# Performance work log

Hardware: AMD Instinct MI355X
Metric: run time of the kernel (lower is better)

Reference implementation:

```python
import jax, jax.numpy as jnp
import numpy as np

BS, C, H, W = 128, 256, 9, 9
D = 9                      # spectral window size
PS = 15                    # padsize
PAD_SPACE = PS - H         # 6
PAD1 = D // 2              # 4 (spectral pad)
START = PAD_SPACE // 2     # 3 (output crop offset)
SPE_HEAD = 25
SHARE_HEAD = 9
SIDE = 5                   # spe_head_Sidelength
BN_EPS = 1e-5


def setup_inputs() -> dict:
    key = jax.random.key(0)
    ks = jax.random.split(key, 12)
    s = 0.1
    return {
        "x": jax.random.normal(ks[0], (BS, C, H, W), jnp.float32),
        "wk": jax.random.normal(ks[1], (H * W, 1, D), jnp.float32) * s,   # depthwise conv1d over spectral axis
        "bk": jax.random.normal(ks[2], (H * W,), jnp.float32) * s,
        "w1": jax.random.normal(ks[3], (SPE_HEAD, SHARE_HEAD, 2 * SHARE_HEAD), jnp.float32) * s,  # grouped 1x1, no bias
        "bn_gamma": jnp.ones((SPE_HEAD * SHARE_HEAD,), jnp.float32),
        "bn_beta": jnp.zeros((SPE_HEAD * SHARE_HEAD,), jnp.float32),
        "bn_mean": jax.random.normal(ks[4], (SPE_HEAD * SHARE_HEAD,), jnp.float32) * s,
        "bn_var": jax.random.uniform(ks[5], (SPE_HEAD * SHARE_HEAD,), jnp.float32, 0.5, 1.5),
        "w2": jax.random.normal(ks[6], (SPE_HEAD, D, SHARE_HEAD), jnp.float32) * s,  # grouped 1x1 -> spe_head*d
        "b2": jax.random.normal(ks[7], (SPE_HEAD * D,), jnp.float32) * s,
        "wv": jax.random.normal(ks[8], (C, 1, 3, 3), jnp.float32) * s,   # depthwise 3x3
        "bv": jax.random.normal(ks[9], (C,), jnp.float32) * s,
    }


def _unfold_k3_d5(t, bs, c):
    # torch nn.Unfold(kernel=3, dilation=5) on a 15x15 map -> 5x5 output positions.
    # row = kh*5 + oh, col = kw*5 + ow, so a plain (3,5,3,5) reshape gives the taps.
    t = t.reshape(bs, c, 3, SIDE, 3, SIDE)              # (bs,c,kh,oh,kw,ow)
    t = t.transpose(0, 1, 2, 4, 3, 5)                   # (bs,c,kh,kw,oh,ow)
    t = t.reshape(bs, c * SHARE_HEAD, SPE_HEAD)          # (bs, c*9, 25) torch unfold layout
    return t.transpose(0, 2, 1)                          # (bs, 25, c*9)


def reference(x, wk, bk, w1, bn_gamma, bn_beta, bn_mean, bn_var, w2, b2, wv, bv):
    bs, c, h, w = x.shape
    # --- key: depthwise conv1d along spectral (channel) axis, one filter per pixel ---
    k = x.reshape(bs, c, h * w).transpose(0, 2, 1)       # (bs, 81, c)
    k1 = jax.lax.conv_general_dilated(
        k, wk, (1,), [(PAD1, PAD1)],
        dimension_numbers=("NCH", "OIH", "NCH"), feature_group_count=h * w,
    ) + bk[None, :, None]                                # (bs, 81, c)
    k1 = k1.transpose(0, 2, 1).reshape(bs, c, h, w)

    # --- pad right/bottom and unfold q, k ---
    k1_pad = jnp.pad(k1, ((0, 0), (0, 0), (0, PAD_SPACE), (0, PAD_SPACE)))  # (bs,c,15,15)
    q_pad = jnp.pad(x, ((0, 0), (0, 0), (0, PAD_SPACE), (0, PAD_SPACE)))
    key_u = _unfold_k3_d5(k1_pad, bs, c)                 # (bs,25,9c)
    q_u = _unfold_k3_d5(q_pad, bs, c)

    # stack + reshape exactly as torch (row-major): (bs,25,2,9c) -> (bs,450,c)
    key_q = jnp.stack((q_u, key_u), axis=2).reshape(bs, 2 * SPE_HEAD * SHARE_HEAD, c)

    # --- attention_embed: grouped 1x1 conv -> BN(eval) -> ReLU -> grouped 1x1 conv ---
    a = jnp.einsum("goi,bgic->bgoc", w1, key_q.reshape(bs, SPE_HEAD, 2 * SHARE_HEAD, c))
    a = a.reshape(bs, SPE_HEAD * SHARE_HEAD, c)          # (bs,225,c)
    inv_std = bn_gamma / jnp.sqrt(bn_var + BN_EPS)
    a = (a - bn_mean[None, :, None]) * inv_std[None, :, None] + bn_beta[None, :, None]
    a = jax.nn.relu(a)
    a = jnp.einsum("goi,bgic->bgoc", w2, a.reshape(bs, SPE_HEAD, SHARE_HEAD, c))
    a = a.reshape(bs, SPE_HEAD * D, c) + b2[None, :, None]  # (bs,225,c)

    # --- build per-pixel spectral kernels: tile, rearrange to 15x15, softmax over d ---
    att = jnp.tile(a.reshape(bs, SPE_HEAD, D, c), (1, SHARE_HEAD, 1, 1))  # (bs,225,9,c)
    att = att.transpose(0, 3, 1, 2)                      # (bs,c,225,d)
    att = att.reshape(bs, c, 3, 3, SIDE, SIDE, D)
    att = att.transpose(0, 1, 2, 4, 3, 5, 6)             # swap dims 3,4 as torch .transpose(3,4)
    att = att.reshape(bs, c, PS, PS, D)
    att = jax.nn.softmax(att, axis=-1)
    att = att.transpose(0, 1, 4, 2, 3)                   # (bs,c,d,15,15)

    # --- value: depthwise 3x3 conv, pad left/top + spectral, sliding window over channels ---
    v = jax.lax.conv_general_dilated(
        x, wv, (1, 1), [(1, 1), (1, 1)],
        dimension_numbers=("NCHW", "OIHW", "NCHW"), feature_group_count=c,
    ) + bv[None, :, None, None]                          # (bs,c,9,9)
    pv = jnp.pad(v, ((0, 0), (PAD1, PAD1), (PAD_SPACE, 0), (PAD_SPACE, 0)))  # (bs,c+8,15,15)
    v_unf = jnp.stack([pv[:, t:t + c] for t in range(D)], axis=2)            # (bs,c,d,15,15)

    out = jnp.sum(v_unf * att, axis=2) + k1_pad          # (bs,c,15,15)
    return out[:, :, START:h + START, START:w + START]    # (bs,c,9,9)
```

## Files before the change

### kernel.cpp

```cpp
#include <hip/hip_runtime.h>

#define C 256
#define HW 81
#define PITCH 292
#define PITCHD 146
#define ZROW 81

typedef __fp16 h2 __attribute__((ext_vector_type(2)));

__device__ __forceinline__ float us2f(unsigned short u) {
  union { unsigned short s; __fp16 h; } c; c.s = u; return (float)c.h;
}
__device__ __forceinline__ float lo_h(unsigned int d) {
  union { unsigned int i; h2 h; } c; c.i = d; return (float)c.h.x;
}
__device__ __forceinline__ float hi_h(unsigned int d) {
  union { unsigned int i; h2 h; } c; c.i = d; return (float)c.h.y;
}
__device__ __forceinline__ unsigned int pkh2(float a, float b) {
  union { h2 h; unsigned int i; } c;
  c.h = __builtin_amdgcn_cvt_pkrtz(a, b);
  return c.i;
}
__device__ __forceinline__ h2 as_h2(unsigned int d) {
  union { unsigned int i; h2 h; } c; c.i = d; return c.h;
}
__device__ __forceinline__ float dot2(unsigned int a, unsigned int b, float c) {
#if __has_builtin(__builtin_amdgcn_fdot2)
  return __builtin_amdgcn_fdot2(as_h2(a), as_h2(b), c, false);
#else
  h2 x = as_h2(a), y = as_h2(b);
  return fmaf((float)x.y, (float)y.y, fmaf((float)x.x, (float)y.x, c));
#endif
}
__device__ __forceinline__ float exp2_fast(float x) {
#if __has_builtin(__builtin_amdgcn_exp2f)
  return __builtin_amdgcn_exp2f(x);
#else
  return __expf(x * 0.6931471805599453f);
#endif
}

__global__ __launch_bounds__(1024) void semca_fused(
    const float* __restrict__ x, const float* __restrict__ wk,
    const float* __restrict__ bk, const float* __restrict__ w1,
    const float* __restrict__ gamma, const float* __restrict__ beta,
    const float* __restrict__ mean, const float* __restrict__ var,
    const float* __restrict__ w2, const float* __restrict__ b2,
    const float* __restrict__ wv, const float* __restrict__ bv,
    float* __restrict__ out) {
  __shared__ unsigned short xT[82 * PITCH];
  __shared__ unsigned short k1T[82 * PITCH];
  __shared__ unsigned short vT[18 * PITCH];
  __shared__ unsigned short pixtab[228];
  __shared__ float2 bnf[225];
  __shared__ unsigned int w1p[225 * 12];
  __shared__ unsigned int w2p[225 * 4];
  __shared__ uint2 wkp[81 * 3];

  const int blk = blockIdx.x;
  const int b = (blk & 7) * 16 + ((blk >> 3) & 15);
  const int s = blk >> 7;
  const int tid = threadIdx.x;
  const float* xb = x + (size_t)b * (C * HW);

  unsigned int* xTd = (unsigned int*)xT;
  unsigned int* k1Td = (unsigned int*)k1T;
  unsigned int* vTd = (unsigned int*)vT;
  unsigned int* wkpd = (unsigned int*)wkp;

  float xe[11], xo[11];
  int adr[11];
  {
    int chp = tid / HW;
    int p = tid - chp * HW;
#pragma unroll
    for (int rep = 0; rep < 10; ++rep) {
      const float* base = xb + (2 * chp) * HW + p;
      xe[rep] = base[0];
      xo[rep] = base[HW];
      adr[rep] = PITCHD * p + 2 + chp;
      chp += 12;
      p += 52;
      if (p >= HW) { p -= HW; chp += 1; }
    }
    if (tid < 128) {
      int f = 10240 + tid;
      int c2 = f / HW, p2 = f - c2 * HW;
      xe[10] = xb[2 * c2 * HW + p2];
      xo[10] = xb[(2 * c2 + 1) * HW + p2];
      adr[10] = PITCHD * p2 + 2 + c2;
    }
  }

  for (int t = tid; t < 810; t += 1024) {
    int p = t / 10, k2 = t - (t / 10) * 10;
    xT[p * PITCH + ((k2 < 4) ? k2 : (256 + k2))] = 0;
  }
  if (tid < PITCHD) {
    xTd[PITCHD * ZROW + tid] = 0;
    k1Td[PITCHD * ZROW + tid] = 0;
  }
  for (int t = tid; t < 225; t += 1024) {
    int g = t / 9, tap = t - (t / 9) * 9;
    int kh = tap / 3, kw = tap - kh * 3;
    int h = kh * 5 + g / 5, w = kw * 5 + (g - (g / 5) * 5);
    pixtab[t] = (h < 9 && w < 9) ? (unsigned short)((h * 9 + w) * PITCH)
                                 : (unsigned short)(ZROW * PITCH);
    float inv = gamma[t] * rsqrtf(var[t] + 1e-5f);
    bnf[t] = make_float2(inv, beta[t] - mean[t] * inv);
  }
  for (int t = tid; t < 2025; t += 1024) {
    int m = t / 9, q = t - m * 9;
    w1p[m * 12 + q] = pkh2(w1[m * 18 + q], w1[m * 18 + 9 + q]);
  }
  if (tid < 900) {
    int m = tid >> 2, j = tid & 3;
    w2p[m * 4 + j] = pkh2(w2[m * 9 + 2 * j], w2[m * 9 + 2 * j + 1]);
  }
  if (tid < 486) {
    int m = tid / 6, j = tid - (tid / 6) * 6;
    const float* wr = wk + m * 9;
    unsigned int v;
    if (j < 4)       v = pkh2(wr[2 * j], wr[2 * j + 1]);
    else if (j == 4) v = pkh2(wr[8], 0.f);
    else             v = pkh2(0.f, wr[8]);
    wkpd[m * 6 + j] = v;
  }

  const int chv = tid & 127;
  float wv_e[9], wv_o[9];
#pragma unroll
  for (int t = 0; t < 9; ++t) {
    wv_e[t] = wv[(2 * chv) * 9 + t];
    wv_o[t] = wv[(2 * chv + 1) * 9 + t];
  }
  const float bv_e = bv[2 * chv], bv_o = bv[2 * chv + 1];

#pragma unroll
  for (int rep = 0; rep < 10; ++rep) xTd[adr[rep]] = pkh2(xe[rep], xo[rep]);
  if (tid < 128) xTd[adr[10]] = pkh2(xe[10], xo[10]);

  __syncthreads();

  {
    auto k1fn = [&](int f) {
      int p = __builtin_amdgcn_readfirstlane(f >> 6);
      int u = f & 63;
      const uint2* wrow2 = (const uint2*)(xTd + PITCHD * p);
      uint2 q0 = wrow2[u], q1 = wrow2[u + 1], q2 = wrow2[u + 2];
      unsigned int D0 = q0.x, D1 = q0.y, D2 = q1.x, D3 = q1.y,
                   D4 = q2.x, D5 = q2.y;
      unsigned int A0 = (D0 >> 16) | (D1 << 16);
      unsigned int A1 = (D1 >> 16) | (D2 << 16);
      unsigned int A2 = (D2 >> 16) | (D3 << 16);
      unsigned int A3 = (D3 >> 16) | (D4 << 16);
      unsigned int A4 = (D4 >> 16) | (D5 << 16);
      const uint2* wkq = wkp + p * 3;
      uint2 wa = wkq[0], wb = wkq[1], wc = wkq[2];
      float bkp = bk[p];
      float c0 = dot2(D0, wa.x, dot2(D1, wa.y, dot2(D2, wb.x,
                 dot2(D3, wb.y, dot2(D4, wc.x, bkp)))));
      float c1 = dot2(A0, wa.x, dot2(A1, wa.y, dot2(A2, wb.x,
                 dot2(A3, wb.y, dot2(D4, wc.y, bkp)))));
      float c2 = dot2(D1, wa.x, dot2(D2, wa.y, dot2(D3, wb.x,
                 dot2(D4, wb.y, dot2(D5, wc.x, bkp)))));
      float c3 = dot2(A1, wa.x, dot2(A2, wa.y, dot2(A3, wb.x,
                 dot2(A4, wb.y, dot2(D5, wc.y, bkp)))));
      *(uint2*)(k1Td + PITCHD * p + 2 + 2 * u) =
          make_uint2(pkh2(c0, c1), pkh2(c2, c3));
    };
#pragma unroll
    for (int rep = 0; rep < 5; ++rep) k1fn(tid + rep * 1024);
    if (tid < 64) k1fn(5120 + tid);
  }

  {
    auto vfn = [&](int f) {
      int e = __builtin_amdgcn_readfirstlane(f >> 7);
      int r0 = e / 6;
      int i = s * 3 + r0;
      int j = e - r0 * 6;
      float a_e = bv_e, a_o = bv_o;
#pragma unroll
      for (int di = 0; di < 3; ++di) {
        int ii = i + di - 1;
        if (ii < 0) continue;
#pragma unroll
        for (int dj = 0; dj < 3; ++dj) {
          int jj = j + dj - 1;
          if (jj < 0) continue;
          unsigned int d = xTd[PITCHD * (ii * 9 + jj) + 2 + chv];
          int t = di * 3 + dj;
          a_e = fmaf(lo_h(d), wv_e[t], a_e);
          a_o = fmaf(hi_h(d), wv_o[t], a_o);
        }
      }
      vTd[PITCHD * e + 2 + chv] = pkh2(a_e, a_o);
    };
#pragma unroll
    for (int rep = 0; rep < 2; ++rep) vfn(tid + rep * 1024);
    if (tid < 256) vfn(2048 + tid);
  }
  if (tid < 180) {
    int e = tid / 10, k2 = tid - (tid / 10) * 10;
    vT[e * PITCH + ((k2 < 4) ? k2 : (256 + k2))] = 0;
  }
  __syncthreads();

  const int s4 = tid >> 8;
  const int ch = tid & 255;
  const int ci0 = ch / 9;
  const int tap0 = ch - ci0 * 9;
  float* outb = out + ((size_t)b * C + ch) * HW;

  int tq[9], cq[9];
  {
    int ci = ci0, tap = tap0;
#pragma unroll
    for (int q = 0; q < 9; ++q) {
      tq[q] = tap;
      cq[q] = 4 + ci;
      tap += 4;
      ci += 28;
      if (tap >= 9) { tap -= 9; ci += 1; }
    }
  }

#define PV_STORE(OH, OW)                                                   \
  do {                                                                     \
    int e_ = gh_i * 6 + ((OW)-3);                                          \
    const unsigned short* vrow_ = vT + e_ * PITCH;                         \
    float acc_ = 0.f;                                                      \
    _Pragma("unroll") for (int d_ = 0; d_ < 9; ++d_) acc_ =                \
        fmaf(a2[d_], us2f(vrow_[ch + d_]), acc_);                          \
    if ((OH) < 6 && (OW) < 6)                                              \
      acc_ = fmaf(acc_, inv_s,                                             \
                  us2f(k1T[(((OH) + 3) * 9 + ((OW) + 3)) * PITCH + 4 + ch])); \
    else                                                                   \
      acc_ *= inv_s;                                                       \
    if (valid_inst) outb[(OH)*9 + (OW)] = acc_;                            \
  } while (0)

#pragma unroll
  for (int k = 0; k < 4; ++k) {
    int idx = s4 * 4 + k;
    const bool valid_inst = (idx < 15);
    if (!valid_inst) idx = 14;
    int gh_i = idx / 5, gw_i = idx - (idx / 5) * 5;
    int oh = (s ? 6 : 3) + gh_i;
    int gh = s ? ((gh_i + 4) % 5) : (gh_i + 1);
    int g9 = __builtin_amdgcn_readfirstlane((gh * 5 + gw_i) * 9);

    unsigned int kqp[9];
#pragma unroll
    for (int q = 0; q < 9; ++q) {
      int off = (int)pixtab[g9 + tq[q]] + cq[q];
      unsigned int xv = xT[off], kv = k1T[off];
      kqp[q] = xv | (kv << 16);
    }

    __builtin_amdgcn_s_setprio(1);
    float r[9];
#pragma unroll
    for (int o = 0; o < 9; ++o) {
      int m = g9 + o;
      const unsigned int* wp = w1p + m * 12;
      float a = 0.f;
#pragma unroll
      for (int q = 0; q < 9; ++q) a = dot2(kqp[q], wp[q], a);
      float2 bn = bnf[m];
      a = fmaf(a, bn.x, bn.y);
      r[o] = fmaxf(a, 0.f);
    }

    unsigned int rp[4];
#pragma unroll
    for (int j = 0; j < 4; ++j) rp[j] = pkh2(r[2 * j], r[2 * j + 1]);
    float a2[9], mx = -1e30f;
#pragma unroll
    for (int d = 0; d < 9; ++d) {
      int m = g9 + d;
      const unsigned int* wq = w2p + m * 4;
      float a = b2[m];
#pragma unroll
      for (int j = 0; j < 4; ++j) a = dot2(rp[j], wq[j], a);
      a = fmaf(w2[m * 9 + 8], r[8], a);
      a2[d] = a;
      mx = fmaxf(mx, a);
    }
    const float L2E = 1.44269504f;
    float nmL = mx * -L2E;
    float ssum = 0.f;
#pragma unroll
    for (int d = 0; d < 9; ++d) {
      a2[d] = exp2_fast(fmaf(a2[d], L2E, nmL));
      ssum += a2[d];
    }
    float inv_s = __builtin_amdgcn_rcpf(ssum);
    __builtin_amdgcn_s_setprio(0);

    int ow0 = (gw_i == 0) ? 7 : (gw_i + 2);
    PV_STORE(oh, ow0);
    if (gw_i == 1) PV_STORE(oh, 8);
  }
#undef PV_STORE

  if (s == 0) {
    if (s4 < 3) {
      int oh = s4;
#pragma unroll
      for (int ow = 0; ow < 9; ++ow) {
        float v2 = 0.f;
        if (ow < 6)
          v2 = us2f(k1T[((oh + 3) * 9 + (ow + 3)) * PITCH + 4 + ch]);
        outb[oh * 9 + ow] = v2;
      }
    } else {
#pragma unroll
      for (int r0 = 0; r0 < 3; ++r0) {
        int oh = 3 + r0;
#pragma unroll
        for (int ow = 0; ow < 3; ++ow)
          outb[oh * 9 + ow] =
              us2f(k1T[((oh + 3) * 9 + (ow + 3)) * PITCH + 4 + ch]);
      }
    }
  } else if (s4 < 3) {
    int oh = 6 + s4;
    outb[oh * 9 + 0] = 0.f;
    outb[oh * 9 + 1] = 0.f;
    outb[oh * 9 + 2] = 0.f;
  }
}

extern "C" void kernel_launch(void* const* d_in, const int* in_sizes, int n_in,
                              void* d_out, int out_size, void* d_ws, size_t ws_size,
                              hipStream_t stream) {
  const float* x     = (const float*)d_in[0];
  const float* wk    = (const float*)d_in[1];
  const float* bk    = (const float*)d_in[2];
  const float* w1    = (const float*)d_in[3];
  const float* gamma = (const float*)d_in[4];
  const float* beta  = (const float*)d_in[5];
  const float* mean  = (const float*)d_in[6];
  const float* var   = (const float*)d_in[7];
  const float* w2    = (const float*)d_in[8];
  const float* b2    = (const float*)d_in[9];
  const float* wv    = (const float*)d_in[10];
  const float* bv    = (const float*)d_in[11];
  float* out = (float*)d_out;

  hipLaunchKernelGGL(semca_fused, dim3(256), dim3(1024), 0, stream,
                     x, wk, bk, w1, gamma, beta, mean, var, w2, b2, wv, bv, out);
}
```

Before: 25.58 us.

## Interleave x and k1 into one LDS array and drop softmax max subtraction

Merges the separate fp16 x and k1 shared-memory tables into one interleaved 32-bit array. Each word now holds an x value in the low half and the matching k1 value in the high half, so the attention stage gets the packed pair with a single LDS load instead of two loads plus a shift and or. The spectral conv is rewritten to use uint4 loads and byte permutes, and it writes k1 into the high halves. Separately, the softmax no longer subtracts the running max before exponentiating, which saves a pass. That risks overflow if the logits get large, though it is safe for the small weights used here.

```diff
diff --git a/kernel.cpp b/kernel.cpp
--- a/kernel.cpp
+++ b/kernel.cpp
@@ -2,8 +2,8 @@
 
 #define C 256
 #define HW 81
+#define XPD 268
 #define PITCH 292
-#define PITCHD 146
 #define ZROW 81
 
 typedef __fp16 h2 __attribute__((ext_vector_type(2)));
@@ -38,6 +38,25 @@
   return __builtin_amdgcn_exp2f(x);
 #else
   return __expf(x * 0.6931471805599453f);
+#endif
+}
+__device__ __forceinline__ unsigned int perm_lo16(unsigned int hi_src,
+                                                  unsigned int lo_src) {
+#if __has_builtin(__builtin_amdgcn_perm)
+  return __builtin_amdgcn_perm(hi_src, lo_src, 0x05040100u);
+#else
+  return (lo_src & 0xffffu) | (hi_src << 16);
+#endif
+}
+__device__ __forceinline__ unsigned int merge_hi(unsigned int h,
+                                                 unsigned int keep_lo,
+                                                 bool use_hi_half) {
+#if __has_builtin(__builtin_amdgcn_perm)
+  return __builtin_amdgcn_perm(h, keep_lo,
+                               use_hi_half ? 0x07060100u : 0x05040100u);
+#else
+  unsigned int hv = use_hi_half ? (h & 0xffff0000u) : (h << 16);
+  return (keep_lo & 0xffffu) | hv;
 #endif
 }
 
@@ -49,8 +68,7 @@
     const float* __restrict__ w2, const float* __restrict__ b2,
     const float* __restrict__ wv, const float* __restrict__ bv,
     float* __restrict__ out) {
-  __shared__ unsigned short xT[82 * PITCH];
-  __shared__ unsigned short k1T[82 * PITCH];
+  __shared__ unsigned int xk1[82 * XPD];
   __shared__ unsigned short vT[18 * PITCH];
   __shared__ unsigned short pixtab[228];
   __shared__ float2 bnf[225];
@@ -64,8 +82,6 @@
   const int tid = threadIdx.x;
   const float* xb = x + (size_t)b * (C * HW);
 
-  unsigned int* xTd = (unsigned int*)xT;
-  unsigned int* k1Td = (unsigned int*)k1T;
   unsigned int* vTd = (unsigned int*)vT;
   unsigned int* wkpd = (unsigned int*)wkp;
 
@@ -79,7 +95,7 @@
       const float* base = xb + (2 * chp) * HW + p;
       xe[rep] = base[0];
       xo[rep] = base[HW];
-      adr[rep] = PITCHD * p + 2 + chp;
+      adr[rep] = XPD * p + 4 + 2 * chp;
       chp += 12;
       p += 52;
       if (p >= HW) { p -= HW; chp += 1; }
@@ -89,24 +105,24 @@
       int c2 = f / HW, p2 = f - c2 * HW;
       xe[10] = xb[2 * c2 * HW + p2];
       xo[10] = xb[(2 * c2 + 1) * HW + p2];
-      adr[10] = PITCHD * p2 + 2 + c2;
-    }
-  }
-
-  for (int t = tid; t < 810; t += 1024) {
-    int p = t / 10, k2 = t - (t / 10) * 10;
-    xT[p * PITCH + ((k2 < 4) ? k2 : (256 + k2))] = 0;
-  }
-  if (tid < PITCHD) {
-    xTd[PITCHD * ZROW + tid] = 0;
-    k1Td[PITCHD * ZROW + tid] = 0;
+      adr[10] = XPD * p2 + 4 + 2 * c2;
+    }
+  }
+
+  for (int t = tid; t < 1240; t += 1024) {
+    if (t < 972) {
+      int row = t / 12, j = t - row * 12;
+      xk1[row * XPD + ((j < 4) ? j : (256 + j))] = 0;
+    } else {
+      xk1[ZROW * XPD + (t - 972)] = 0;
+    }
   }
   for (int t = tid; t < 225; t += 1024) {
     int g = t / 9, tap = t - (t / 9) * 9;
     int kh = tap / 3, kw = tap - kh * 3;
     int h = kh * 5 + g / 5, w = kw * 5 + (g - (g / 5) * 5);
-    pixtab[t] = (h < 9 && w < 9) ? (unsigned short)((h * 9 + w) * PITCH)
-                                 : (unsigned short)(ZROW * PITCH);
+    pixtab[t] = (h < 9 && w < 9) ? (unsigned short)((h * 9 + w) * XPD)
+                                 : (unsigned short)(ZROW * XPD);
     float inv = gamma[t] * rsqrtf(var[t] + 1e-5f);
     bnf[t] = make_float2(inv, beta[t] - mean[t] * inv);
   }
@@ -138,8 +154,12 @@
   const float bv_e = bv[2 * chv], bv_o = bv[2 * chv + 1];
 
 #pragma unroll
-  for (int rep = 0; rep < 10; ++rep) xTd[adr[rep]] = pkh2(xe[rep], xo[rep]);
-  if (tid < 128) xTd[adr[10]] = pkh2(xe[10], xo[10]);
+  for (int rep = 0; rep < 10; ++rep)
+    *(uint2*)(xk1 + adr[rep]) =
+        make_uint2(pkh2(xe[rep], 0.f), pkh2(xo[rep], 0.f));
+  if (tid < 128)
+    *(uint2*)(xk1 + adr[10]) =
+        make_uint2(pkh2(xe[10], 0.f), pkh2(xo[10], 0.f));
 
   __syncthreads();
 
@@ -147,28 +167,31 @@
     auto k1fn = [&](int f) {
       int p = __builtin_amdgcn_readfirstlane(f >> 6);
       int u = f & 63;
-      const uint2* wrow2 = (const uint2*)(xTd + PITCHD * p);
-      uint2 q0 = wrow2[u], q1 = wrow2[u + 1], q2 = wrow2[u + 2];
-      unsigned int D0 = q0.x, D1 = q0.y, D2 = q1.x, D3 = q1.y,
-                   D4 = q2.x, D5 = q2.y;
-      unsigned int A0 = (D0 >> 16) | (D1 << 16);
-      unsigned int A1 = (D1 >> 16) | (D2 << 16);
-      unsigned int A2 = (D2 >> 16) | (D3 << 16);
-      unsigned int A3 = (D3 >> 16) | (D4 << 16);
-      unsigned int A4 = (D4 >> 16) | (D5 << 16);
+      const uint4* W4 = (const uint4*)(xk1 + XPD * p + 4 * u);
+      uint4 A = W4[0], B = W4[1], Cq = W4[2];
+      unsigned int W[12] = {A.x, A.y, A.z, A.w, B.x, B.y,
+                            B.z, B.w, Cq.x, Cq.y, Cq.z, Cq.w};
+      unsigned int P[11];
+#pragma unroll
+      for (int i = 0; i < 11; ++i) P[i] = perm_lo16(W[i + 1], W[i]);
       const uint2* wkq = wkp + p * 3;
       uint2 wa = wkq[0], wb = wkq[1], wc = wkq[2];
       float bkp = bk[p];
-      float c0 = dot2(D0, wa.x, dot2(D1, wa.y, dot2(D2, wb.x,
-                 dot2(D3, wb.y, dot2(D4, wc.x, bkp)))));
-      float c1 = dot2(A0, wa.x, dot2(A1, wa.y, dot2(A2, wb.x,
-                 dot2(A3, wb.y, dot2(D4, wc.y, bkp)))));
-      float c2 = dot2(D1, wa.x, dot2(D2, wa.y, dot2(D3, wb.x,
-                 dot2(D4, wb.y, dot2(D5, wc.x, bkp)))));
-      float c3 = dot2(A1, wa.x, dot2(A2, wa.y, dot2(A3, wb.x,
-                 dot2(A4, wb.y, dot2(D5, wc.y, bkp)))));
-      *(uint2*)(k1Td + PITCHD * p + 2 + 2 * u) =
-          make_uint2(pkh2(c0, c1), pkh2(c2, c3));
+      float c0 = dot2(P[0], wa.x, dot2(P[2], wa.y, dot2(P[4], wb.x,
+                 dot2(P[6], wb.y, dot2(P[8], wc.x, bkp)))));
+      float c1 = dot2(P[1], wa.x, dot2(P[3], wa.y, dot2(P[5], wb.x,
+                 dot2(P[7], wb.y, dot2(P[9], wc.x, bkp)))));
+      float c2 = dot2(P[2], wa.x, dot2(P[4], wa.y, dot2(P[6], wb.x,
+                 dot2(P[8], wb.y, dot2(P[10], wc.x, bkp)))));
+      float c3 = dot2(P[3], wa.x, dot2(P[5], wa.y, dot2(P[7], wb.x,
+                 dot2(P[9], wb.y, dot2(P[10], wc.y, bkp)))));
+      unsigned int h01 = pkh2(c0, c1), h23 = pkh2(c2, c3);
+      uint4 o;
+      o.x = merge_hi(h01, B.x, false);
+      o.y = merge_hi(h01, B.y, true);
+      o.z = merge_hi(h23, B.z, false);
+      o.w = merge_hi(h23, B.w, true);
+      *(uint4*)(xk1 + XPD * p + 4 + 4 * u) = o;
     };
 #pragma unroll
     for (int rep = 0; rep < 5; ++rep) k1fn(tid + rep * 1024);
@@ -190,13 +213,13 @@
         for (int dj = 0; dj < 3; ++dj) {
           int jj = j + dj - 1;
           if (jj < 0) continue;
-          unsigned int d = xTd[PITCHD * (ii * 9 + jj) + 2 + chv];
+          uint2 d = *(const uint2*)(xk1 + XPD * (ii * 9 + jj) + 4 + 2 * chv);
           int t = di * 3 + dj;
-          a_e = fmaf(lo_h(d), wv_e[t], a_e);
-          a_o = fmaf(hi_h(d), wv_o[t], a_o);
+          a_e = fmaf(lo_h(d.x), wv_e[t], a_e);
+          a_o = fmaf(lo_h(d.y), wv_o[t], a_o);
         }
       }
-      vTd[PITCHD * e + 2 + chv] = pkh2(a_e, a_o);
+      vTd[(PITCH / 2) * e + 2 + chv] = pkh2(a_e, a_o);
     };
 #pragma unroll
     for (int rep = 0; rep < 2; ++rep) vfn(tid + rep * 1024);
@@ -236,7 +259,7 @@
         fmaf(a2[d_], us2f(vrow_[ch + d_]), acc_);                          \
     if ((OH) < 6 && (OW) < 6)                                              \
       acc_ = fmaf(acc_, inv_s,                                             \
-                  us2f(k1T[(((OH) + 3) * 9 + ((OW) + 3)) * PITCH + 4 + ch])); \
+                  hi_h(xk1[XPD * (((OH) + 3) * 9 + ((OW) + 3)) + 4 + ch])); \
     else                                                                   \
       acc_ *= inv_s;                                                       \
     if (valid_inst) outb[(OH)*9 + (OW)] = acc_;                            \
@@ -254,11 +277,8 @@
 
     unsigned int kqp[9];
 #pragma unroll
-    for (int q = 0; q < 9; ++q) {
-      int off = (int)pixtab[g9 + tq[q]] + cq[q];
-      unsigned int xv = xT[off], kv = k1T[off];
-      kqp[q] = xv | (kv << 16);
-    }
+    for (int q = 0; q < 9; ++q)
+      kqp[q] = xk1[(int)pixtab[g9 + tq[q]] + cq[q]];
 
     __builtin_amdgcn_s_setprio(1);
     float r[9];
@@ -277,7 +297,8 @@
     unsigned int rp[4];
 #pragma unroll
     for (int j = 0; j < 4; ++j) rp[j] = pkh2(r[2 * j], r[2 * j + 1]);
-    float a2[9], mx = -1e30f;
+    const float L2E = 1.44269504f;
+    float a2[9], ssum = 0.f;
 #pragma unroll
     for (int d = 0; d < 9; ++d) {
       int m = g9 + d;
@@ -286,15 +307,7 @@
 #pragma unroll
       for (int j = 0; j < 4; ++j) a = dot2(rp[j], wq[j], a);
       a = fmaf(w2[m * 9 + 8], r[8], a);
-      a2[d] = a;
-      mx = fmaxf(mx, a);
-    }
-    const float L2E = 1.44269504f;
-    float nmL = mx * -L2E;
-    float ssum = 0.f;
-#pragma unroll
-    for (int d = 0; d < 9; ++d) {
-      a2[d] = exp2_fast(fmaf(a2[d], L2E, nmL));
+      a2[d] = exp2_fast(a * L2E);
       ssum += a2[d];
     }
     float inv_s = __builtin_amdgcn_rcpf(ssum);
@@ -313,7 +326,7 @@
       for (int ow = 0; ow < 9; ++ow) {
         float v2 = 0.f;
         if (ow < 6)
-          v2 = us2f(k1T[((oh + 3) * 9 + (ow + 3)) * PITCH + 4 + ch]);
+          v2 = hi_h(xk1[XPD * ((oh + 3) * 9 + (ow + 3)) + 4 + ch]);
         outb[oh * 9 + ow] = v2;
       }
     } else {
@@ -323,7 +336,7 @@
 #pragma unroll
         for (int ow = 0; ow < 3; ++ow)
           outb[oh * 9 + ow] =
-              us2f(k1T[((oh + 3) * 9 + (ow + 3)) * PITCH + 4 + ch]);
+              hi_h(xk1[XPD * ((oh + 3) * 9 + (ow + 3)) + 4 + ch]);
       }
     }
   } else if (s4 < 3) {
```

New measurement: 25.92 us. No clear change (+1.3%).

## Compute k1 only for needed pixels and widen per-thread work to eight outputs

Applied to the files above, without the earlier changes.

The key conv1d stage now computes eight spectral outputs per thread, with overlapping words reused in registers, instead of four. It also restricts the computed pixels to the rows each block slice s actually needs (rows 1-8 for s==0, a subset of rows otherwise) instead of all 81. The aim is to cut redundant LDS reads and arithmetic in that stage. The risk is that some pixel rows are skipped when they are needed, and that the imbalanced thread counts may leave lanes idle.

```diff
diff --git a/kernel.cpp b/kernel.cpp
--- a/kernel.cpp
+++ b/kernel.cpp
@@ -144,35 +144,54 @@
   __syncthreads();
 
   {
-    auto k1fn = [&](int f) {
-      int p = __builtin_amdgcn_readfirstlane(f >> 6);
-      int u = f & 63;
-      const uint2* wrow2 = (const uint2*)(xTd + PITCHD * p);
-      uint2 q0 = wrow2[u], q1 = wrow2[u + 1], q2 = wrow2[u + 2];
-      unsigned int D0 = q0.x, D1 = q0.y, D2 = q1.x, D3 = q1.y,
-                   D4 = q2.x, D5 = q2.y;
-      unsigned int A0 = (D0 >> 16) | (D1 << 16);
-      unsigned int A1 = (D1 >> 16) | (D2 << 16);
-      unsigned int A2 = (D2 >> 16) | (D3 << 16);
-      unsigned int A3 = (D3 >> 16) | (D4 << 16);
-      unsigned int A4 = (D4 >> 16) | (D5 << 16);
+    auto k1fn8 = [&](int p, int oct) {
+      const uint2* wrow2 = (const uint2*)(xTd + PITCHD * p + 4 * oct);
+      uint2 r0 = wrow2[0], r1 = wrow2[1], r2 = wrow2[2], r3 = wrow2[3];
+      unsigned int W[8] = {r0.x, r0.y, r1.x, r1.y, r2.x, r2.y, r3.x, r3.y};
+      unsigned int A[7];
+#pragma unroll
+      for (int k2 = 0; k2 < 7; ++k2)
+        A[k2] = (W[k2] >> 16) | (W[k2 + 1] << 16);
       const uint2* wkq = wkp + p * 3;
       uint2 wa = wkq[0], wb = wkq[1], wc = wkq[2];
       float bkp = bk[p];
-      float c0 = dot2(D0, wa.x, dot2(D1, wa.y, dot2(D2, wb.x,
-                 dot2(D3, wb.y, dot2(D4, wc.x, bkp)))));
-      float c1 = dot2(A0, wa.x, dot2(A1, wa.y, dot2(A2, wb.x,
-                 dot2(A3, wb.y, dot2(D4, wc.y, bkp)))));
-      float c2 = dot2(D1, wa.x, dot2(D2, wa.y, dot2(D3, wb.x,
-                 dot2(D4, wb.y, dot2(D5, wc.x, bkp)))));
-      float c3 = dot2(A1, wa.x, dot2(A2, wa.y, dot2(A3, wb.x,
-                 dot2(A4, wb.y, dot2(D5, wc.y, bkp)))));
-      *(uint2*)(k1Td + PITCHD * p + 2 + 2 * u) =
-          make_uint2(pkh2(c0, c1), pkh2(c2, c3));
+      float cc[8];
+#pragma unroll
+      for (int j2 = 0; j2 < 4; ++j2) {
+        cc[2 * j2] =
+            dot2(W[j2], wa.x, dot2(W[j2 + 1], wa.y, dot2(W[j2 + 2], wb.x,
+            dot2(W[j2 + 3], wb.y, dot2(W[j2 + 4], wc.x, bkp)))));
+        cc[2 * j2 + 1] =
+            dot2(A[j2], wa.x, dot2(A[j2 + 1], wa.y, dot2(A[j2 + 2], wb.x,
+            dot2(A[j2 + 3], wb.y, dot2(W[j2 + 4], wc.y, bkp)))));
+      }
+      unsigned int* dst = k1Td + PITCHD * p + 2 + 4 * oct;
+      *(uint2*)dst = make_uint2(pkh2(cc[0], cc[1]), pkh2(cc[2], cc[3]));
+      *(uint2*)(dst + 2) = make_uint2(pkh2(cc[4], cc[5]), pkh2(cc[6], cc[7]));
     };
-#pragma unroll
-    for (int rep = 0; rep < 5; ++rep) k1fn(tid + rep * 1024);
-    if (tid < 64) k1fn(5120 + tid);
+    if (s == 0) {
+#pragma unroll
+      for (int rep = 0; rep < 2; ++rep) {
+        int f = tid + rep * 1024;
+        k1fn8(9 + (f >> 5), f & 31);
+      }
+      if (tid < 256) {
+        int f = 2048 + tid;
+        k1fn8(9 + (f >> 5), f & 31);
+      }
+    } else {
+      auto prow = [&](int f) {
+        int idx = f >> 5;
+        int ri = idx / 9, col = idx - ri * 9;
+        int row = ri + ((ri >= 2) ? 2 : 0);
+        return row * 9 + col;
+      };
+      k1fn8(prow(tid), tid & 31);
+      if (tid < 416) {
+        int f = 1024 + tid;
+        k1fn8(prow(f), f & 31);
+      }
+    }
   }
 
   {
```

Result: no change. 25.27 us (-1.2%).
